# Performance work log

Hardware: AMD Instinct MI355X
Metric: run time of the kernel (lower is better)

The kernel has to match this reference:

```python
import jax, jax.numpy as jnp
import numpy as np

NUM_CLUSTERS = 32
EPS = 1e-12

def _l2norm(v, axis):
    return v / jnp.maximum(jnp.linalg.norm(v, axis=axis, keepdims=True), EPS)

def setup_inputs() -> dict:
    key = jax.random.key(0)
    k1, k2, k3 = jax.random.split(key, 3)
    B, M, D, K = 64, 512, 2048, NUM_CLUSTERS
    init_sc = 1.0 / np.sqrt(D)
    x = jax.random.normal(k1, (B, M, D), dtype=jnp.float32)
    W = init_sc * jax.random.normal(k2, (K, D), dtype=jnp.float32)
    centroids = init_sc * jax.random.normal(k3, (K, D), dtype=jnp.float32)
    return {"x": x, "W": W, "centroids": centroids}

def reference(x, W, centroids):
    # x: [B, M, D] frame features; W: [K, D]; centroids: [K, D]
    xn = _l2norm(x, axis=-1)                              # per-frame L2 normalize
    sa = jax.nn.softmax(jnp.einsum('bmd,kd->bmk', xn, W), axis=-1)  # [B, M, K]
    # vlad[b,k,d] = sum_m sa[b,m,k] * (xn[b,m,d] - centroids[k,d])
    #            = (sa^T @ xn)[b,k,d] - colsum(sa)[b,k] * centroids[k,d]
    agg = jnp.einsum('bmk,bmd->bkd', sa, xn)              # [B, K, D]
    vlad = agg - jnp.sum(sa, axis=1)[..., None] * centroids[None]
    vlad = _l2norm(vlad, axis=2)                          # intra-normalize per cluster
    vlad = vlad.reshape(vlad.shape[0], -1)                # [B, K*D]
    return _l2norm(vlad, axis=1)
```

## Files before the change

kernel.cpp:

```cpp
#include <hip/hip_runtime.h>
#include <hip/hip_bf16.h>
#include <cstdint>
#include <cstddef>

#define Bn 64
#define Mn 512
#define Dn 2048
#define Kn 32
#define EPSF 1e-12f

typedef __attribute__((ext_vector_type(8))) __bf16 bf16x8;
typedef __attribute__((ext_vector_type(4))) __bf16 bf16x4;
typedef __attribute__((ext_vector_type(4))) float f32x4;

__global__ __launch_bounds__(256) void k0_wcvt(const float* __restrict__ W,
                                               __bf16* __restrict__ wbf) {
  int i = (blockIdx.x * 256 + threadIdx.x) * 4;
  f32x4 v = *(const f32x4*)(W + i);
  bf16x4 o;
  o[0] = (__bf16)v[0]; o[1] = (__bf16)v[1]; o[2] = (__bf16)v[2]; o[3] = (__bf16)v[3];
  *(bf16x4*)(wbf + i) = o;
}

template <bool XBF>
__global__ __launch_bounds__(256, 4) void k1_logits_softmax(const float* __restrict__ x,
                                                            const __bf16* __restrict__ Wb,
                                                            __bf16* __restrict__ saT,
                                                            float* __restrict__ colsum,
                                                            __bf16* __restrict__ xbf) {
  __shared__ float red[2][64][9];
  int wv = threadIdx.x >> 6, lane = threadIdx.x & 63;
  int g = wv & 1, h = wv >> 1;
  int mr = lane & 15, q = lane >> 4;
  int blk = blockIdx.x;
  int row0 = blk * 32 + g * 16;
  int b = blk >> 4;
  const float* xp = x + (size_t)(row0 + mr) * Dn + h * 1024 + q * 8;
  const __bf16* wp0 = Wb + (size_t)mr * Dn + h * 1024 + q * 8;
  const __bf16* wp1 = Wb + (size_t)(mr + 16) * Dn + h * 1024 + q * 8;
  __bf16* xs = XBF ? (xbf + (size_t)(row0 + mr) * Dn + h * 1024 + q * 8) : nullptr;
  f32x4 acc0 = {0.f, 0.f, 0.f, 0.f};
  f32x4 acc1 = {0.f, 0.f, 0.f, 0.f};
  float ssq = 0.f;
#pragma unroll 2
  for (int s = 0; s < 32; ++s) {
    f32x4 xa = *(const f32x4*)(xp + s * 32);
    f32x4 xb = *(const f32x4*)(xp + s * 32 + 4);
    bf16x8 b0 = *(const bf16x8*)(wp0 + s * 32);
    bf16x8 b1 = *(const bf16x8*)(wp1 + s * 32);
    bf16x8 af;
    af[0] = (__bf16)xa[0]; af[1] = (__bf16)xa[1];
    af[2] = (__bf16)xa[2]; af[3] = (__bf16)xa[3];
    af[4] = (__bf16)xb[0]; af[5] = (__bf16)xb[1];
    af[6] = (__bf16)xb[2]; af[7] = (__bf16)xb[3];
    if constexpr (XBF) *(bf16x8*)(xs + s * 32) = af;
    ssq = fmaf(xa[0], xa[0], ssq); ssq = fmaf(xa[1], xa[1], ssq);
    ssq = fmaf(xa[2], xa[2], ssq); ssq = fmaf(xa[3], xa[3], ssq);
    ssq = fmaf(xb[0], xb[0], ssq); ssq = fmaf(xb[1], xb[1], ssq);
    ssq = fmaf(xb[2], xb[2], ssq); ssq = fmaf(xb[3], xb[3], ssq);
    acc0 = __builtin_amdgcn_mfma_f32_16x16x32_bf16(af, b0, acc0, 0, 0, 0);
    acc1 = __builtin_amdgcn_mfma_f32_16x16x32_bf16(af, b1, acc1, 0, 0, 0);
  }
  if (h == 1) {
#pragma unroll
    for (int r = 0; r < 4; ++r) { red[g][lane][r] = acc0[r]; red[g][lane][4 + r] = acc1[r]; }
    red[g][lane][8] = ssq;
  }
  __syncthreads();
  if (h == 1) return;
#pragma unroll
  for (int r = 0; r < 4; ++r) { acc0[r] += red[g][lane][r]; acc1[r] += red[g][lane][4 + r]; }
  ssq += red[g][lane][8];
  ssq += __shfl_xor(ssq, 16);
  ssq += __shfl_xor(ssq, 32);
  float invb = 1.f / fmaxf(sqrtf(ssq), EPSF);
  float cs0 = 0.f, cs1 = 0.f;
  bf16x4 v40, v41;
#pragma unroll
  for (int r = 0; r < 4; ++r) {
    float inv = __shfl(invb, q * 4 + r);
    float v0 = acc0[r] * inv, v1 = acc1[r] * inv;
    float mx = fmaxf(v0, v1);
    mx = fmaxf(mx, __shfl_xor(mx, 1));
    mx = fmaxf(mx, __shfl_xor(mx, 2));
    mx = fmaxf(mx, __shfl_xor(mx, 4));
    mx = fmaxf(mx, __shfl_xor(mx, 8));
    float e0 = __expf(v0 - mx), e1 = __expf(v1 - mx);
    float sm = e0 + e1;
    sm += __shfl_xor(sm, 1); sm += __shfl_xor(sm, 2);
    sm += __shfl_xor(sm, 4); sm += __shfl_xor(sm, 8);
    float rs = 1.f / sm;
    float sa0 = e0 * rs, sa1 = e1 * rs;
    v40[r] = (__bf16)(sa0 * inv);
    v41[r] = (__bf16)(sa1 * inv);
    cs0 += sa0; cs1 += sa1;
  }
  int mloc = row0 & 511;
  __bf16* st = saT + ((size_t)(b * Kn + mr)) * Mn + mloc + q * 4;
  *(bf16x4*)st = v40;
  *(bf16x4*)(st + (size_t)16 * Mn) = v41;
  cs0 += __shfl_xor(cs0, 16); cs0 += __shfl_xor(cs0, 32);
  cs1 += __shfl_xor(cs1, 16); cs1 += __shfl_xor(cs1, 32);
  if (lane < 16) {
    atomicAdd(&colsum[b * Kn + mr], cs0);
    atomicAdd(&colsum[b * Kn + mr + 16], cs1);
  }
}

template <bool XBF>
__global__ __launch_bounds__(256, 6) void k3_agg(const float* __restrict__ x,
                                                 const __bf16* __restrict__ xbf,
                                                 const __bf16* __restrict__ saT,
                                                 const float* __restrict__ colsum,
                                                 const float* __restrict__ cent,
                                                 float* __restrict__ vlad,
                                                 float* __restrict__ ssq) {
  __shared__ __bf16 tile[2][Kn][40];
  __shared__ float csl[Kn];
  int b = blockIdx.x >> 5;
  int chunk = blockIdx.x & 31;
  int t = threadIdx.x;
  int w = t >> 6, lane = t & 63;
  int n = lane & 15, q = lane >> 4;
  int d0 = chunk * 64 + w * 16;
  int sk = t >> 3, mo = (t & 7) * 4;
  const __bf16* sg = saT + ((size_t)b * Kn + sk) * Mn + mo;
  if (t < Kn) csl[t] = colsum[b * Kn + t];
  *(bf16x4*)&tile[0][sk][mo] = *(const bf16x4*)sg;
  const float* xgf = x + (size_t)b * Mn * Dn + d0 + n;
  const __bf16* xgb = XBF ? (xbf + (size_t)b * Mn * Dn + d0 + n) : nullptr;
  f32x4 acc[2] = {};
  for (int it = 0; it < 16; ++it) {
    int m0 = it * 32;
    int cb = it & 1;
    __syncthreads();
    bf16x4 stg = {};
    if (it < 15) stg = *(const bf16x4*)(sg + m0 + 32);
    bf16x8 bv;
    if constexpr (XBF) {
      const __bf16* xp = xgb + (size_t)(m0 + q * 8) * Dn;
#pragma unroll
      for (int j = 0; j < 8; ++j) bv[j] = xp[(size_t)j * Dn];
    } else {
      const float* xp = xgf + (size_t)(m0 + q * 8) * Dn;
#pragma unroll
      for (int j = 0; j < 8; ++j) bv[j] = (__bf16)xp[(size_t)j * Dn];
    }
    bf16x8 a0 = *(const bf16x8*)&tile[cb][n][q * 8];
    bf16x8 a1 = *(const bf16x8*)&tile[cb][n + 16][q * 8];
    acc[0] = __builtin_amdgcn_mfma_f32_16x16x32_bf16(a0, bv, acc[0], 0, 0, 0);
    acc[1] = __builtin_amdgcn_mfma_f32_16x16x32_bf16(a1, bv, acc[1], 0, 0, 0);
    if (it < 15) *(bf16x4*)&tile[cb ^ 1][sk][mo] = stg;
  }
  const float* cg = cent + d0 + n;
#pragma unroll
  for (int kt = 0; kt < 2; ++kt) {
#pragma unroll
    for (int r = 0; r < 4; ++r) {
      int k = kt * 16 + q * 4 + r;
      float vv = acc[kt][r] - csl[k] * cg[(size_t)k * Dn];
      vlad[((size_t)(b * Kn + k)) * Dn + d0 + n] = vv;
      float sq = vv * vv;
      sq += __shfl_xor(sq, 1); sq += __shfl_xor(sq, 2);
      sq += __shfl_xor(sq, 4); sq += __shfl_xor(sq, 8);
      if (n == 0) atomicAdd(&ssq[b * Kn + k], sq);
    }
  }
}

__global__ __launch_bounds__(256) void k4_norm(float* __restrict__ out,
                                               const float* __restrict__ ssq) {
  __shared__ float rk[Kn];
  __shared__ float us[Kn];
  int b = blockIdx.x >> 4;
  int t = threadIdx.x;
  if (t < Kn) {
    float ss = ssq[b * Kn + t];
    float r = 1.f / fmaxf(sqrtf(ss), EPSF);
    rk[t] = r;
    us[t] = ss * r * r;
  }
  __syncthreads();
  float S = 0.f;
#pragma unroll
  for (int k = 0; k < Kn; ++k) S += us[k];
  float s = 1.f / fmaxf(sqrtf(S), EPSF);
  int chunk = blockIdx.x & 15;
  size_t base = (size_t)b * (Kn * Dn) + (size_t)chunk * 4096;
  f32x4* p = (f32x4*)(out + base);
#pragma unroll
  for (int i = 0; i < 4; ++i) {
    int idx = t + 256 * i;
    int k = (chunk * 4096 + idx * 4) >> 11;
    f32x4 v = p[idx];
    float sc = rk[k] * s;
    v[0] *= sc; v[1] *= sc; v[2] *= sc; v[3] *= sc;
    p[idx] = v;
  }
}

extern "C" void kernel_launch(void* const* d_in, const int* in_sizes, int n_in,
                              void* d_out, int out_size, void* d_ws, size_t ws_size,
                              hipStream_t stream) {
  const float* x = (const float*)d_in[0];
  const float* W = (const float*)d_in[1];
  const float* cent = (const float*)d_in[2];
  float* out = (float*)d_out;
  char* ws = (char*)d_ws;
  float* colsum = (float*)ws;
  float* ssqb = (float*)(ws + 8192);
  __bf16* wbf = (__bf16*)(ws + 16384);
  __bf16* saT = (__bf16*)(ws + 16384 + 131072);
  __bf16* xbf = (__bf16*)(ws + 16384 + 131072 + 2097152);
  size_t need_xbf = 16384 + 131072 + 2097152 + (size_t)Bn * Mn * Dn * 2;
  bool use_xbf = ws_size >= need_xbf;
  hipMemsetAsync(ws, 0, 16384, stream);
  k0_wcvt<<<dim3(64), dim3(256), 0, stream>>>(W, wbf);
  if (use_xbf) {
    k1_logits_softmax<true><<<dim3(1024), dim3(256), 0, stream>>>(x, wbf, saT, colsum, xbf);
    k3_agg<true><<<dim3(2048), dim3(256), 0, stream>>>(x, xbf, saT, colsum, cent, out, ssqb);
  } else {
    k1_logits_softmax<false><<<dim3(1024), dim3(256), 0, stream>>>(x, wbf, saT, colsum, nullptr);
    k3_agg<false><<<dim3(2048), dim3(256), 0, stream>>>(x, nullptr, saT, colsum, cent, out, ssqb);
  }
  k4_norm<<<dim3(1024), dim3(256), 0, stream>>>(out, ssqb);
}
```

Before: 446.6 us.

## Drop bf16 x staging, fuse final normalization into aggregation via last-block counter

Removes the bf16 copy of x written by the logits kernel, so the aggregation kernel reads the fp32 x directly. Also reverses block order in the logits kernel so the most recently read x rows are likely still in the L2/LLC when aggregation starts. Replaces the separate normalization kernel with a per-batch atomic completion counter: the last aggregation block for each batch does the intra and global L2 scaling. It also splits the sum-of-squares accumulator into two chains. The costs are more fp32 traffic in aggregation and a serial tail where a single block scales 64K floats per batch.

```diff
diff --git a/kernel.cpp b/kernel.cpp
--- a/kernel.cpp
+++ b/kernel.cpp
@@ -22,26 +22,23 @@
   *(bf16x4*)(wbf + i) = o;
 }
 
-template <bool XBF>
 __global__ __launch_bounds__(256, 4) void k1_logits_softmax(const float* __restrict__ x,
                                                             const __bf16* __restrict__ Wb,
                                                             __bf16* __restrict__ saT,
-                                                            float* __restrict__ colsum,
-                                                            __bf16* __restrict__ xbf) {
+                                                            float* __restrict__ colsum) {
   __shared__ float red[2][64][9];
   int wv = threadIdx.x >> 6, lane = threadIdx.x & 63;
   int g = wv & 1, h = wv >> 1;
   int mr = lane & 15, q = lane >> 4;
-  int blk = blockIdx.x;
+  int blk = 1023 - blockIdx.x;
   int row0 = blk * 32 + g * 16;
   int b = blk >> 4;
   const float* xp = x + (size_t)(row0 + mr) * Dn + h * 1024 + q * 8;
   const __bf16* wp0 = Wb + (size_t)mr * Dn + h * 1024 + q * 8;
   const __bf16* wp1 = Wb + (size_t)(mr + 16) * Dn + h * 1024 + q * 8;
-  __bf16* xs = XBF ? (xbf + (size_t)(row0 + mr) * Dn + h * 1024 + q * 8) : nullptr;
   f32x4 acc0 = {0.f, 0.f, 0.f, 0.f};
   f32x4 acc1 = {0.f, 0.f, 0.f, 0.f};
-  float ssq = 0.f;
+  float sqa = 0.f, sqb = 0.f;
 #pragma unroll 2
   for (int s = 0; s < 32; ++s) {
     f32x4 xa = *(const f32x4*)(xp + s * 32);
@@ -53,14 +50,14 @@
     af[2] = (__bf16)xa[2]; af[3] = (__bf16)xa[3];
     af[4] = (__bf16)xb[0]; af[5] = (__bf16)xb[1];
     af[6] = (__bf16)xb[2]; af[7] = (__bf16)xb[3];
-    if constexpr (XBF) *(bf16x8*)(xs + s * 32) = af;
-    ssq = fmaf(xa[0], xa[0], ssq); ssq = fmaf(xa[1], xa[1], ssq);
-    ssq = fmaf(xa[2], xa[2], ssq); ssq = fmaf(xa[3], xa[3], ssq);
-    ssq = fmaf(xb[0], xb[0], ssq); ssq = fmaf(xb[1], xb[1], ssq);
-    ssq = fmaf(xb[2], xb[2], ssq); ssq = fmaf(xb[3], xb[3], ssq);
+    sqa = fmaf(xa[0], xa[0], sqa); sqb = fmaf(xa[1], xa[1], sqb);
+    sqa = fmaf(xa[2], xa[2], sqa); sqb = fmaf(xa[3], xa[3], sqb);
+    sqa = fmaf(xb[0], xb[0], sqa); sqb = fmaf(xb[1], xb[1], sqb);
+    sqa = fmaf(xb[2], xb[2], sqa); sqb = fmaf(xb[3], xb[3], sqb);
     acc0 = __builtin_amdgcn_mfma_f32_16x16x32_bf16(af, b0, acc0, 0, 0, 0);
     acc1 = __builtin_amdgcn_mfma_f32_16x16x32_bf16(af, b1, acc1, 0, 0, 0);
   }
+  float ssq = sqa + sqb;
   if (h == 1) {
 #pragma unroll
     for (int r = 0; r < 4; ++r) { red[g][lane][r] = acc0[r]; red[g][lane][4 + r] = acc1[r]; }
@@ -107,16 +104,17 @@
   }
 }
 
-template <bool XBF>
 __global__ __launch_bounds__(256, 6) void k3_agg(const float* __restrict__ x,
-                                                 const __bf16* __restrict__ xbf,
                                                  const __bf16* __restrict__ saT,
                                                  const float* __restrict__ colsum,
                                                  const float* __restrict__ cent,
                                                  float* __restrict__ vlad,
-                                                 float* __restrict__ ssq) {
+                                                 float* __restrict__ ssq,
+                                                 unsigned int* __restrict__ done) {
   __shared__ __bf16 tile[2][Kn][40];
   __shared__ float csl[Kn];
+  __shared__ int winner;
+  __shared__ float rk2[Kn], us2[Kn];
   int b = blockIdx.x >> 5;
   int chunk = blockIdx.x & 31;
   int t = threadIdx.x;
@@ -128,7 +126,6 @@
   if (t < Kn) csl[t] = colsum[b * Kn + t];
   *(bf16x4*)&tile[0][sk][mo] = *(const bf16x4*)sg;
   const float* xgf = x + (size_t)b * Mn * Dn + d0 + n;
-  const __bf16* xgb = XBF ? (xbf + (size_t)b * Mn * Dn + d0 + n) : nullptr;
   f32x4 acc[2] = {};
   for (int it = 0; it < 16; ++it) {
     int m0 = it * 32;
@@ -136,16 +133,10 @@
     __syncthreads();
     bf16x4 stg = {};
     if (it < 15) stg = *(const bf16x4*)(sg + m0 + 32);
+    const float* xp = xgf + (size_t)(m0 + q * 8) * Dn;
     bf16x8 bv;
-    if constexpr (XBF) {
-      const __bf16* xp = xgb + (size_t)(m0 + q * 8) * Dn;
-#pragma unroll
-      for (int j = 0; j < 8; ++j) bv[j] = xp[(size_t)j * Dn];
-    } else {
-      const float* xp = xgf + (size_t)(m0 + q * 8) * Dn;
-#pragma unroll
-      for (int j = 0; j < 8; ++j) bv[j] = (__bf16)xp[(size_t)j * Dn];
-    }
+#pragma unroll
+    for (int j = 0; j < 8; ++j) bv[j] = (__bf16)xp[(size_t)j * Dn];
     bf16x8 a0 = *(const bf16x8*)&tile[cb][n][q * 8];
     bf16x8 a1 = *(const bf16x8*)&tile[cb][n + 16][q * 8];
     acc[0] = __builtin_amdgcn_mfma_f32_16x16x32_bf16(a0, bv, acc[0], 0, 0, 0);
@@ -166,34 +157,34 @@
       if (n == 0) atomicAdd(&ssq[b * Kn + k], sq);
     }
   }
-}
-
-__global__ __launch_bounds__(256) void k4_norm(float* __restrict__ out,
-                                               const float* __restrict__ ssq) {
-  __shared__ float rk[Kn];
-  __shared__ float us[Kn];
-  int b = blockIdx.x >> 4;
-  int t = threadIdx.x;
+  __threadfence();
+  if (t == 0) {
+    unsigned int prev = __hip_atomic_fetch_add(&done[b], 1u, __ATOMIC_ACQ_REL,
+                                               __HIP_MEMORY_SCOPE_AGENT);
+    winner = (prev == 31);
+  }
+  __syncthreads();
+  if (!winner) return;
+  __threadfence();
   if (t < Kn) {
-    float ss = ssq[b * Kn + t];
+    float ss = __hip_atomic_load(&ssq[b * Kn + t], __ATOMIC_RELAXED,
+                                 __HIP_MEMORY_SCOPE_AGENT);
     float r = 1.f / fmaxf(sqrtf(ss), EPSF);
-    rk[t] = r;
-    us[t] = ss * r * r;
+    rk2[t] = r;
+    us2[t] = ss * r * r;
   }
   __syncthreads();
   float S = 0.f;
 #pragma unroll
-  for (int k = 0; k < Kn; ++k) S += us[k];
+  for (int k = 0; k < Kn; ++k) S += us2[k];
   float s = 1.f / fmaxf(sqrtf(S), EPSF);
-  int chunk = blockIdx.x & 15;
-  size_t base = (size_t)b * (Kn * Dn) + (size_t)chunk * 4096;
-  f32x4* p = (f32x4*)(out + base);
-#pragma unroll
-  for (int i = 0; i < 4; ++i) {
+  f32x4* p = (f32x4*)(vlad + (size_t)b * (Kn * Dn));
+#pragma unroll 4
+  for (int i = 0; i < 64; ++i) {
     int idx = t + 256 * i;
-    int k = (chunk * 4096 + idx * 4) >> 11;
+    int k = idx >> 9;
     f32x4 v = p[idx];
-    float sc = rk[k] * s;
+    float sc = rk2[k] * s;
     v[0] *= sc; v[1] *= sc; v[2] *= sc; v[3] *= sc;
     p[idx] = v;
   }
@@ -209,19 +200,11 @@
   char* ws = (char*)d_ws;
   float* colsum = (float*)ws;
   float* ssqb = (float*)(ws + 8192);
-  __bf16* wbf = (__bf16*)(ws + 16384);
-  __bf16* saT = (__bf16*)(ws + 16384 + 131072);
-  __bf16* xbf = (__bf16*)(ws + 16384 + 131072 + 2097152);
-  size_t need_xbf = 16384 + 131072 + 2097152 + (size_t)Bn * Mn * Dn * 2;
-  bool use_xbf = ws_size >= need_xbf;
-  hipMemsetAsync(ws, 0, 16384, stream);
+  unsigned int* done = (unsigned int*)(ws + 16384);
+  __bf16* wbf = (__bf16*)(ws + 32768);
+  __bf16* saT = (__bf16*)(ws + 32768 + 131072);
+  hipMemsetAsync(ws, 0, 32768, stream);
   k0_wcvt<<<dim3(64), dim3(256), 0, stream>>>(W, wbf);
-  if (use_xbf) {
-    k1_logits_softmax<true><<<dim3(1024), dim3(256), 0, stream>>>(x, wbf, saT, colsum, xbf);
-    k3_agg<true><<<dim3(2048), dim3(256), 0, stream>>>(x, xbf, saT, colsum, cent, out, ssqb);
-  } else {
-    k1_logits_softmax<false><<<dim3(1024), dim3(256), 0, stream>>>(x, wbf, saT, colsum, nullptr);
-    k3_agg<false><<<dim3(2048), dim3(256), 0, stream>>>(x, nullptr, saT, colsum, cent, out, ssqb);
-  }
-  k4_norm<<<dim3(1024), dim3(256), 0, stream>>>(out, ssqb);
-}
+  k1_logits_softmax<<<dim3(1024), dim3(256), 0, stream>>>(x, wbf, saT, colsum);
+  k3_agg<<<dim3(2048), dim3(256), 0, stream>>>(x, saT, colsum, cent, out, ssqb, done);
+}
```

Measured after the change: 903.2 us. 102% more time.

## Drop bf16 x copy, stage full assignment tile in LDS, stagger access phases

Applied to the files above, without the earlier changes.

Removes the intermediate bf16 copy of x: k1 no longer writes it, and k3 reads the fp32 x directly, converting it in registers. k3 now loads the whole per-batch soft-assignment matrix into padded LDS once instead of double-buffering 32-column slices with a barrier each iteration. Both kernels rotate their loop start per block to spread DRAM/L2 accesses, and k1 walks blocks in reverse, presumably so k3 finds recently touched x in cache. The aim is to cut the 128MB bf16 write and the per-iteration syncs, at the cost of k3 reading fp32 x (twice the bytes of the bf16 copy) and using more LDS, which lowers occupancy.

```diff
diff --git a/kernel.cpp b/kernel.cpp
--- a/kernel.cpp
+++ b/kernel.cpp
@@ -22,45 +22,44 @@
   *(bf16x4*)(wbf + i) = o;
 }
 
-template <bool XBF>
 __global__ __launch_bounds__(256, 4) void k1_logits_softmax(const float* __restrict__ x,
                                                             const __bf16* __restrict__ Wb,
                                                             __bf16* __restrict__ saT,
-                                                            float* __restrict__ colsum,
-                                                            __bf16* __restrict__ xbf) {
+                                                            float* __restrict__ colsum) {
   __shared__ float red[2][64][9];
   int wv = threadIdx.x >> 6, lane = threadIdx.x & 63;
   int g = wv & 1, h = wv >> 1;
   int mr = lane & 15, q = lane >> 4;
-  int blk = blockIdx.x;
+  int blk = 1023 - blockIdx.x;
+  int ph = (blk * 5) & 31;
   int row0 = blk * 32 + g * 16;
   int b = blk >> 4;
   const float* xp = x + (size_t)(row0 + mr) * Dn + h * 1024 + q * 8;
   const __bf16* wp0 = Wb + (size_t)mr * Dn + h * 1024 + q * 8;
   const __bf16* wp1 = Wb + (size_t)(mr + 16) * Dn + h * 1024 + q * 8;
-  __bf16* xs = XBF ? (xbf + (size_t)(row0 + mr) * Dn + h * 1024 + q * 8) : nullptr;
   f32x4 acc0 = {0.f, 0.f, 0.f, 0.f};
   f32x4 acc1 = {0.f, 0.f, 0.f, 0.f};
-  float ssq = 0.f;
+  float sqa = 0.f, sqb = 0.f;
 #pragma unroll 2
   for (int s = 0; s < 32; ++s) {
-    f32x4 xa = *(const f32x4*)(xp + s * 32);
-    f32x4 xb = *(const f32x4*)(xp + s * 32 + 4);
-    bf16x8 b0 = *(const bf16x8*)(wp0 + s * 32);
-    bf16x8 b1 = *(const bf16x8*)(wp1 + s * 32);
+    int s2 = (s + ph) & 31;
+    f32x4 xa = *(const f32x4*)(xp + s2 * 32);
+    f32x4 xb = *(const f32x4*)(xp + s2 * 32 + 4);
+    bf16x8 b0 = *(const bf16x8*)(wp0 + s2 * 32);
+    bf16x8 b1 = *(const bf16x8*)(wp1 + s2 * 32);
     bf16x8 af;
     af[0] = (__bf16)xa[0]; af[1] = (__bf16)xa[1];
     af[2] = (__bf16)xa[2]; af[3] = (__bf16)xa[3];
     af[4] = (__bf16)xb[0]; af[5] = (__bf16)xb[1];
     af[6] = (__bf16)xb[2]; af[7] = (__bf16)xb[3];
-    if constexpr (XBF) *(bf16x8*)(xs + s * 32) = af;
-    ssq = fmaf(xa[0], xa[0], ssq); ssq = fmaf(xa[1], xa[1], ssq);
-    ssq = fmaf(xa[2], xa[2], ssq); ssq = fmaf(xa[3], xa[3], ssq);
-    ssq = fmaf(xb[0], xb[0], ssq); ssq = fmaf(xb[1], xb[1], ssq);
-    ssq = fmaf(xb[2], xb[2], ssq); ssq = fmaf(xb[3], xb[3], ssq);
+    sqa = fmaf(xa[0], xa[0], sqa); sqb = fmaf(xa[1], xa[1], sqb);
+    sqa = fmaf(xa[2], xa[2], sqa); sqb = fmaf(xa[3], xa[3], sqb);
+    sqa = fmaf(xb[0], xb[0], sqa); sqb = fmaf(xb[1], xb[1], sqb);
+    sqa = fmaf(xb[2], xb[2], sqa); sqb = fmaf(xb[3], xb[3], sqb);
     acc0 = __builtin_amdgcn_mfma_f32_16x16x32_bf16(af, b0, acc0, 0, 0, 0);
     acc1 = __builtin_amdgcn_mfma_f32_16x16x32_bf16(af, b1, acc1, 0, 0, 0);
   }
+  float ssq = sqa + sqb;
   if (h == 1) {
 #pragma unroll
     for (int r = 0; r < 4; ++r) { red[g][lane][r] = acc0[r]; red[g][lane][4 + r] = acc1[r]; }
@@ -107,50 +106,43 @@
   }
 }
 
-template <bool XBF>
-__global__ __launch_bounds__(256, 6) void k3_agg(const float* __restrict__ x,
-                                                 const __bf16* __restrict__ xbf,
+#define AS 520
+__global__ __launch_bounds__(256, 4) void k3_agg(const float* __restrict__ x,
                                                  const __bf16* __restrict__ saT,
                                                  const float* __restrict__ colsum,
                                                  const float* __restrict__ cent,
                                                  float* __restrict__ vlad,
                                                  float* __restrict__ ssq) {
-  __shared__ __bf16 tile[2][Kn][40];
+  __shared__ __bf16 sal[Kn * AS];
   __shared__ float csl[Kn];
   int b = blockIdx.x >> 5;
   int chunk = blockIdx.x & 31;
+  int ph = (blockIdx.x * 5) & 15;
   int t = threadIdx.x;
+  const __bf16* sg = saT + (size_t)b * Kn * Mn;
+#pragma unroll
+  for (int i = 0; i < 8; ++i) {
+    int u = t + 256 * i;
+    int kr = u >> 6, off = (u & 63) * 8;
+    *(bf16x8*)&sal[kr * AS + off] = *(const bf16x8*)(sg + (size_t)kr * Mn + off);
+  }
+  if (t < Kn) csl[t] = colsum[b * Kn + t];
+  __syncthreads();
   int w = t >> 6, lane = t & 63;
   int n = lane & 15, q = lane >> 4;
   int d0 = chunk * 64 + w * 16;
-  int sk = t >> 3, mo = (t & 7) * 4;
-  const __bf16* sg = saT + ((size_t)b * Kn + sk) * Mn + mo;
-  if (t < Kn) csl[t] = colsum[b * Kn + t];
-  *(bf16x4*)&tile[0][sk][mo] = *(const bf16x4*)sg;
-  const float* xgf = x + (size_t)b * Mn * Dn + d0 + n;
-  const __bf16* xgb = XBF ? (xbf + (size_t)b * Mn * Dn + d0 + n) : nullptr;
+  const float* xg = x + (size_t)b * Mn * Dn + d0 + n;
   f32x4 acc[2] = {};
   for (int it = 0; it < 16; ++it) {
-    int m0 = it * 32;
-    int cb = it & 1;
-    __syncthreads();
-    bf16x4 stg = {};
-    if (it < 15) stg = *(const bf16x4*)(sg + m0 + 32);
+    int m0 = ((it + ph) & 15) * 32;
+    bf16x8 a0 = *(const bf16x8*)&sal[n * AS + m0 + q * 8];
+    bf16x8 a1 = *(const bf16x8*)&sal[(n + 16) * AS + m0 + q * 8];
+    const float* xp = xg + (size_t)(m0 + q * 8) * Dn;
     bf16x8 bv;
-    if constexpr (XBF) {
-      const __bf16* xp = xgb + (size_t)(m0 + q * 8) * Dn;
-#pragma unroll
-      for (int j = 0; j < 8; ++j) bv[j] = xp[(size_t)j * Dn];
-    } else {
-      const float* xp = xgf + (size_t)(m0 + q * 8) * Dn;
-#pragma unroll
-      for (int j = 0; j < 8; ++j) bv[j] = (__bf16)xp[(size_t)j * Dn];
-    }
-    bf16x8 a0 = *(const bf16x8*)&tile[cb][n][q * 8];
-    bf16x8 a1 = *(const bf16x8*)&tile[cb][n + 16][q * 8];
+#pragma unroll
+    for (int j = 0; j < 8; ++j) bv[j] = (__bf16)xp[(size_t)j * Dn];
     acc[0] = __builtin_amdgcn_mfma_f32_16x16x32_bf16(a0, bv, acc[0], 0, 0, 0);
     acc[1] = __builtin_amdgcn_mfma_f32_16x16x32_bf16(a1, bv, acc[1], 0, 0, 0);
-    if (it < 15) *(bf16x4*)&tile[cb ^ 1][sk][mo] = stg;
   }
   const float* cg = cent + d0 + n;
 #pragma unroll
@@ -211,17 +203,9 @@
   float* ssqb = (float*)(ws + 8192);
   __bf16* wbf = (__bf16*)(ws + 16384);
   __bf16* saT = (__bf16*)(ws + 16384 + 131072);
-  __bf16* xbf = (__bf16*)(ws + 16384 + 131072 + 2097152);
-  size_t need_xbf = 16384 + 131072 + 2097152 + (size_t)Bn * Mn * Dn * 2;
-  bool use_xbf = ws_size >= need_xbf;
   hipMemsetAsync(ws, 0, 16384, stream);
   k0_wcvt<<<dim3(64), dim3(256), 0, stream>>>(W, wbf);
-  if (use_xbf) {
-    k1_logits_softmax<true><<<dim3(1024), dim3(256), 0, stream>>>(x, wbf, saT, colsum, xbf);
-    k3_agg<true><<<dim3(2048), dim3(256), 0, stream>>>(x, xbf, saT, colsum, cent, out, ssqb);
-  } else {
-    k1_logits_softmax<false><<<dim3(1024), dim3(256), 0, stream>>>(x, wbf, saT, colsum, nullptr);
-    k3_agg<false><<<dim3(2048), dim3(256), 0, stream>>>(x, nullptr, saT, colsum, cent, out, ssqb);
-  }
+  k1_logits_softmax<<<dim3(1024), dim3(256), 0, stream>>>(x, wbf, saT, colsum);
+  k3_agg<<<dim3(2048), dim3(256), 0, stream>>>(x, saT, colsum, cent, out, ssqb);
   k4_norm<<<dim3(1024), dim3(256), 0, stream>>>(out, ssqb);
 }
```

After: 447.4 us. Within noise of the previous version (+0.2%).
